# Performance work log

Hardware: AMD Instinct MI355X
Metric: run time of the kernel (lower is better)

## Reference

```python
import jax, jax.numpy as jnp
import numpy as np

B, T, H, LD = 32, 2048, 1024, 1024

def setup_inputs() -> dict:
    key = jax.random.key(0)
    k1, k2, k3, k4, k5 = jax.random.split(key, 5)
    scale = 1.0 / np.sqrt(H)
    return {
        "encoder_hidden": jax.random.normal(k1, (B, T, H), dtype=jnp.float32),
        "decoder_hidden": jax.random.normal(k2, (B, H), dtype=jnp.float32),
        "W1": jax.random.normal(k3, (H, LD), dtype=jnp.float32) * scale,
        "b1": jnp.zeros((LD,), dtype=jnp.float32),
        "W2": jax.random.normal(k4, (H, LD), dtype=jnp.float32) * scale,
        "b2": jnp.zeros((LD,), dtype=jnp.float32),
        "V": jax.random.normal(k5, (LD, 1), dtype=jnp.float32) * (1.0 / np.sqrt(LD)),
        "bV": jnp.zeros((1,), dtype=jnp.float32),
    }

def reference(encoder_hidden, decoder_hidden, W1, b1, W2, b2, V, bV):
    # dec proj: [B, 1, ld]
    dec_w = (decoder_hidden @ W1 + b1)[:, None, :]
    # enc proj: [B, T, ld]
    enc_w = jnp.einsum('bth,hl->btl', encoder_hidden, W2) + b2
    # multiplicative combine (as in source: decoder_Weight * encoder_weight)
    score = jnp.tanh(dec_w * enc_w) @ V + bV          # [B, T, 1]
    attn = jax.nn.softmax(score, axis=1)              # softmax over time
    context = jnp.sum(attn * encoder_hidden, axis=1)  # [B, H]
    return context, attn
```

## Files before the change

### kernel.cpp

```cpp
#include <hip/hip_runtime.h>
#include <hip/hip_bf16.h>
#include <math.h>

#define B_  32
#define T_  2048
#define H_  1024
#define LD_ 1024
#define M_  (B_*T_)

typedef __attribute__((ext_vector_type(8))) short bf16x8;
typedef __attribute__((ext_vector_type(4))) float f32x4;

__device__ __forceinline__ void async_copy16(void* lds, const void* g) {
  __builtin_amdgcn_global_load_lds(
      (const __attribute__((address_space(1))) void*)g,
      (__attribute__((address_space(3))) void*)lds, 16, 0, 0);
}

__global__ void convert_w2(const float* __restrict__ W2, __hip_bfloat16* __restrict__ w2p) {
  int idx = blockIdx.x * 256 + threadIdx.x;
  int kg = idx >> 10, n = idx & 1023;
  __align__(16) __hip_bfloat16 h[8];
#pragma unroll
  for (int j = 0; j < 8; ++j)
    h[j] = __float2bfloat16(W2[(size_t)(kg * 8 + j) * LD_ + n]);
  *reinterpret_cast<uint4*>(&w2p[(size_t)kg * (LD_ * 8) + n * 8]) =
      *reinterpret_cast<const uint4*>(h);
}

__global__ void dec_proj(const float* __restrict__ dec, const float* __restrict__ W1,
                         const float* __restrict__ b1, float* __restrict__ dec_w) {
  __shared__ float sdec[H_];
  int bb = blockIdx.x >> 2;
  int l = (blockIdx.x & 3) * 256 + threadIdx.x;
  for (int i = threadIdx.x; i < H_; i += 256) sdec[i] = dec[bb * H_ + i];
  __syncthreads();
  float a0 = 0.f, a1 = 0.f, a2 = 0.f, a3 = 0.f;
  for (int h = 0; h < H_; h += 4) {
    a0 += sdec[h + 0] * W1[(h + 0) * LD_ + l];
    a1 += sdec[h + 1] * W1[(h + 1) * LD_ + l];
    a2 += sdec[h + 2] * W1[(h + 2) * LD_ + l];
    a3 += sdec[h + 3] * W1[(h + 3) * LD_ + l];
  }
  dec_w[bb * LD_ + l] = (a0 + a1) + (a2 + a3) + b1[l];
}

__global__ __launch_bounds__(256, 2)
void score_gemm(const float* __restrict__ enc,
                const __hip_bfloat16* __restrict__ w2p,
                const float* __restrict__ dec_w,
                const float* __restrict__ b2,
                const float* __restrict__ V,
                float* __restrict__ score) {
  __shared__ __align__(16) __hip_bfloat16 Bsm[2][8][256][8];

  const int tid  = threadIdx.x;
  const int lane = tid & 63;
  const int wave = tid >> 6;
  const int wm = wave >> 1, wn = wave & 1;
  const int bid = blockIdx.y * gridDim.x + blockIdx.x;
  const int swz = (bid & 7) * 256 + (bid >> 3);
  const int mb = swz >> 2, nb = swz & 3;
  const int row0 = mb * 128, col0 = nb * 256;
  const int q = lane >> 4, c15 = lane & 15;

  f32x4 acc[4][8] = {};

  const float* abase = enc + (size_t)(row0 + wm * 64 + c15) * H_ + q * 8;

  float4 ap[4][2];

  auto ALOAD = [&](int k0) {
#pragma unroll
    for (int i = 0; i < 4; ++i) {
      const float4* s = reinterpret_cast<const float4*>(abase + (size_t)i * 16 * H_ + k0);
      ap[i][0] = s[0];
      ap[i][1] = s[1];
    }
  };
  auto ACVT = [&](bf16x8* af) {
#pragma unroll
    for (int i = 0; i < 4; ++i) {
      __align__(16) __hip_bfloat16 h[8];
      h[0] = __float2bfloat16(ap[i][0].x); h[1] = __float2bfloat16(ap[i][0].y);
      h[2] = __float2bfloat16(ap[i][0].z); h[3] = __float2bfloat16(ap[i][0].w);
      h[4] = __float2bfloat16(ap[i][1].x); h[5] = __float2bfloat16(ap[i][1].y);
      h[6] = __float2bfloat16(ap[i][1].z); h[7] = __float2bfloat16(ap[i][1].w);
      af[i] = *reinterpret_cast<const bf16x8*>(h);
    }
  };
  auto GLOADB = [&](int buf, int k0) {
    char* bbase = (char*)&Bsm[buf][0][0][0] + tid * 16;
    const char* gbase = (const char*)w2p + ((size_t)(k0 >> 3)) * (LD_ * 8 * 2)
                        + (size_t)col0 * 16 + tid * 16;
#pragma unroll
    for (int p = 0; p < 8; ++p)
      async_copy16(bbase + p * 4096, gbase + (size_t)p * (LD_ * 8 * 2));
  };

  GLOADB(0, 0);
  ALOAD(0);
  __syncthreads();

  for (int t = 0; t < 16; ++t) {
    const int cur = t & 1;
    const int k0 = t * 64;
    bf16x8 af[4], bfr[8];

    ACVT(af);
    ALOAD(k0 + 32);
    if (t < 15) GLOADB(cur ^ 1, k0 + 64);
#pragma unroll
    for (int j = 0; j < 8; ++j)
      bfr[j] = *reinterpret_cast<const bf16x8*>(&Bsm[cur][q][wn * 128 + j * 16 + c15][0]);
#pragma unroll
    for (int i = 0; i < 4; ++i)
#pragma unroll
      for (int j = 0; j < 8; ++j)
        acc[i][j] = __builtin_amdgcn_mfma_f32_16x16x32_bf16(af[i], bfr[j], acc[i][j], 0, 0, 0);

    ACVT(af);
    if (t < 15) ALOAD(k0 + 64);
#pragma unroll
    for (int j = 0; j < 8; ++j)
      bfr[j] = *reinterpret_cast<const bf16x8*>(&Bsm[cur][q + 4][wn * 128 + j * 16 + c15][0]);
#pragma unroll
    for (int i = 0; i < 4; ++i)
#pragma unroll
      for (int j = 0; j < 8; ++j)
        acc[i][j] = __builtin_amdgcn_mfma_f32_16x16x32_bf16(af[i], bfr[j], acc[i][j], 0, 0, 0);

    __syncthreads();
  }

  const int bb = row0 >> 11;
  float b2v[8], dwv[8], Vv[8];
#pragma unroll
  for (int j = 0; j < 8; ++j) {
    int n = col0 + wn * 128 + j * 16 + c15;
    b2v[j] = b2[n];
    dwv[j] = dec_w[bb * LD_ + n];
    Vv[j]  = V[n];
  }
#pragma unroll
  for (int i = 0; i < 4; ++i) {
#pragma unroll
    for (int r = 0; r < 4; ++r) {
      float v = 0.f;
#pragma unroll
      for (int j = 0; j < 8; ++j) {
        float e = acc[i][j][r] + b2v[j];
        v += tanhf(dwv[j] * e) * Vv[j];
      }
      v += __shfl_xor(v, 1);
      v += __shfl_xor(v, 2);
      v += __shfl_xor(v, 4);
      v += __shfl_xor(v, 8);
      if (c15 == 0) {
        int row = row0 + wm * 64 + i * 16 + q * 4 + r;
        atomicAdd(&score[row], v);
      }
    }
  }
}

__global__ void softmax_k(const float* __restrict__ score, float* __restrict__ attn) {
  int bb = blockIdx.x;
  int tid = threadIdx.x;
  int lane = tid & 63, wave = tid >> 6;
  __shared__ float red[4];
  float v[8];
  float mx = -3.4e38f;
#pragma unroll
  for (int i = 0; i < 8; ++i) {
    v[i] = score[bb * T_ + i * 256 + tid];
    mx = fmaxf(mx, v[i]);
  }
#pragma unroll
  for (int m = 32; m >= 1; m >>= 1) mx = fmaxf(mx, __shfl_xor(mx, m));
  if (lane == 0) red[wave] = mx;
  __syncthreads();
  mx = fmaxf(fmaxf(red[0], red[1]), fmaxf(red[2], red[3]));
  __syncthreads();
  float s = 0.f;
#pragma unroll
  for (int i = 0; i < 8; ++i) { v[i] = __expf(v[i] - mx); s += v[i]; }
#pragma unroll
  for (int m = 32; m >= 1; m >>= 1) s += __shfl_xor(s, m);
  if (lane == 0) red[wave] = s;
  __syncthreads();
  s = red[0] + red[1] + red[2] + red[3];
  float inv = 1.f / s;
#pragma unroll
  for (int i = 0; i < 8; ++i) attn[bb * T_ + i * 256 + tid] = v[i] * inv;
}

__global__ __launch_bounds__(256)
void context_k(const float* __restrict__ enc, const float* __restrict__ attn,
               float* __restrict__ ctx) {
  const int bb = blockIdx.y;
  const int t0 = blockIdx.x * 128;
  __shared__ float sat[128];
  if (threadIdx.x < 128) sat[threadIdx.x] = attn[bb * T_ + t0 + threadIdx.x];
  __syncthreads();
  const float4* base = reinterpret_cast<const float4*>(
      enc + ((size_t)bb * T_ + t0) * H_) + threadIdx.x;
  f32x4 a0 = {}, a1 = {}, a2 = {}, a3 = {};
  for (int t = 0; t < 128; t += 8) {
    float4 v[8];
#pragma unroll
    for (int u = 0; u < 8; ++u) v[u] = base[(size_t)(t + u) * (H_ / 4)];
#pragma unroll
    for (int u = 0; u < 8; ++u) {
      float a = sat[t + u];
      f32x4& d = (u & 2) ? ((u & 1) ? a3 : a2) : ((u & 1) ? a1 : a0);
      d[0] += a * v[u].x; d[1] += a * v[u].y;
      d[2] += a * v[u].z; d[3] += a * v[u].w;
    }
  }
  const int h = threadIdx.x * 4;
  atomicAdd(&ctx[bb * H_ + h + 0], (a0[0] + a1[0]) + (a2[0] + a3[0]));
  atomicAdd(&ctx[bb * H_ + h + 1], (a0[1] + a1[1]) + (a2[1] + a3[1]));
  atomicAdd(&ctx[bb * H_ + h + 2], (a0[2] + a1[2]) + (a2[2] + a3[2]));
  atomicAdd(&ctx[bb * H_ + h + 3], (a0[3] + a1[3]) + (a2[3] + a3[3]));
}

extern "C" void kernel_launch(void* const* d_in, const int* in_sizes, int n_in,
                              void* d_out, int out_size, void* d_ws, size_t ws_size,
                              hipStream_t stream) {
  const float* enc = (const float*)d_in[0];
  const float* dec = (const float*)d_in[1];
  const float* W1  = (const float*)d_in[2];
  const float* b1  = (const float*)d_in[3];
  const float* W2  = (const float*)d_in[4];
  const float* b2  = (const float*)d_in[5];
  const float* V   = (const float*)d_in[6];

  char* ws = (char*)d_ws;
  __hip_bfloat16* w2p = (__hip_bfloat16*)ws;
  float* dec_w = (float*)(ws + (2u << 20));
  float* score = (float*)(ws + (2u << 20) + (128u << 10));

  float* out  = (float*)d_out;
  float* ctx  = out;
  float* attn = out + B_ * H_;

  hipMemsetAsync(score, 0, (size_t)M_ * sizeof(float), stream);
  hipMemsetAsync(ctx, 0, (size_t)B_ * H_ * sizeof(float), stream);

  convert_w2<<<(H_ * LD_ / 8) / 256, 256, 0, stream>>>(W2, w2p);
  dec_proj<<<B_ * 4, 256, 0, stream>>>(dec, W1, b1, dec_w);
  score_gemm<<<dim3(LD_ / 256, M_ / 128), 256, 0, stream>>>(enc, w2p, dec_w, b2, V, score);
  softmax_k<<<B_, 256, 0, stream>>>(score, attn);
  context_k<<<dim3(16, B_), 256, 0, stream>>>(enc, attn, ctx);
}
```

Before: 720.6 us.

## Pre-convert encoder to packed bf16 and load GEMM operands directly from global

Adds a convert_enc pre-pass that writes the encoder activations as bf16 in an MFMA-fragment-friendly packed layout into workspace, when the workspace is large enough. The score GEMM then reads both A and B fragments straight from global memory into registers with a two-stage register double buffer, and drops the LDS staging and per-iteration barriers. The intent is to halve A-side bytes re-read by the four column blocks and to remove in-loop conversion and synchronisation. The cost is an extra full pass over the 256MB encoder tensor plus a 128MB write. Direct global fragment loads may also get less reuse than LDS staging.

```diff
diff --git a/kernel.cpp b/kernel.cpp
--- a/kernel.cpp
+++ b/kernel.cpp
@@ -11,12 +11,6 @@
 typedef __attribute__((ext_vector_type(8))) short bf16x8;
 typedef __attribute__((ext_vector_type(4))) float f32x4;
 
-__device__ __forceinline__ void async_copy16(void* lds, const void* g) {
-  __builtin_amdgcn_global_load_lds(
-      (const __attribute__((address_space(1))) void*)g,
-      (__attribute__((address_space(3))) void*)lds, 16, 0, 0);
-}
-
 __global__ void convert_w2(const float* __restrict__ W2, __hip_bfloat16* __restrict__ w2p) {
   int idx = blockIdx.x * 256 + threadIdx.x;
   int kg = idx >> 10, n = idx & 1023;
@@ -26,6 +20,32 @@
     h[j] = __float2bfloat16(W2[(size_t)(kg * 8 + j) * LD_ + n]);
   *reinterpret_cast<uint4*>(&w2p[(size_t)kg * (LD_ * 8) + n * 8]) =
       *reinterpret_cast<const uint4*>(h);
+}
+
+__global__ __launch_bounds__(256)
+void convert_enc(const float* __restrict__ enc, __hip_bfloat16* __restrict__ encp) {
+  __shared__ __hip_bfloat16 sb[16][H_ + 8];
+  const int rb = blockIdx.x;
+  const int tid = threadIdx.x;
+  const float4* src = reinterpret_cast<const float4*>(enc + (size_t)rb * 16 * H_);
+#pragma unroll
+  for (int p = 0; p < 16; ++p) {
+    int idx = p * 256 + tid;
+    int r = idx >> 8, c4 = idx & 255;
+    float4 f = src[idx];
+    __align__(8) __hip_bfloat16 h[4];
+    h[0] = __float2bfloat16(f.x); h[1] = __float2bfloat16(f.y);
+    h[2] = __float2bfloat16(f.z); h[3] = __float2bfloat16(f.w);
+    *reinterpret_cast<uint2*>(&sb[r][c4 * 4]) = *reinterpret_cast<const uint2*>(h);
+  }
+  __syncthreads();
+  uint4* dst = reinterpret_cast<uint4*>((char*)encp + (size_t)rb * 32768);
+#pragma unroll
+  for (int p = 0; p < 8; ++p) {
+    int c = p * 256 + tid;
+    int kg = c >> 4, rlow = c & 15;
+    dst[c] = *reinterpret_cast<const uint4*>(&sb[rlow][kg * 8]);
+  }
 }
 
 __global__ void dec_proj(const float* __restrict__ dec, const float* __restrict__ W1,
@@ -45,20 +65,20 @@
   dec_w[bb * LD_ + l] = (a0 + a1) + (a2 + a3) + b1[l];
 }
 
+template<bool BF16A>
 __global__ __launch_bounds__(256, 2)
 void score_gemm(const float* __restrict__ enc,
+                const __hip_bfloat16* __restrict__ encp,
                 const __hip_bfloat16* __restrict__ w2p,
                 const float* __restrict__ dec_w,
                 const float* __restrict__ b2,
                 const float* __restrict__ V,
                 float* __restrict__ score) {
-  __shared__ __align__(16) __hip_bfloat16 Bsm[2][8][256][8];
-
   const int tid  = threadIdx.x;
   const int lane = tid & 63;
   const int wave = tid >> 6;
   const int wm = wave >> 1, wn = wave & 1;
-  const int bid = blockIdx.y * gridDim.x + blockIdx.x;
+  const int bid = blockIdx.x;
   const int swz = (bid & 7) * 256 + (bid >> 3);
   const int mb = swz >> 2, nb = swz & 3;
   const int row0 = mb * 128, col0 = nb * 256;
@@ -66,71 +86,63 @@
 
   f32x4 acc[4][8] = {};
 
-  const float* abase = enc + (size_t)(row0 + wm * 64 + c15) * H_ + q * 8;
-
-  float4 ap[4][2];
-
-  auto ALOAD = [&](int k0) {
-#pragma unroll
-    for (int i = 0; i < 4; ++i) {
-      const float4* s = reinterpret_cast<const float4*>(abase + (size_t)i * 16 * H_ + k0);
-      ap[i][0] = s[0];
-      ap[i][1] = s[1];
-    }
-  };
-  auto ACVT = [&](bf16x8* af) {
-#pragma unroll
-    for (int i = 0; i < 4; ++i) {
-      __align__(16) __hip_bfloat16 h[8];
-      h[0] = __float2bfloat16(ap[i][0].x); h[1] = __float2bfloat16(ap[i][0].y);
-      h[2] = __float2bfloat16(ap[i][0].z); h[3] = __float2bfloat16(ap[i][0].w);
-      h[4] = __float2bfloat16(ap[i][1].x); h[5] = __float2bfloat16(ap[i][1].y);
-      h[6] = __float2bfloat16(ap[i][1].z); h[7] = __float2bfloat16(ap[i][1].w);
-      af[i] = *reinterpret_cast<const bf16x8*>(h);
-    }
-  };
-  auto GLOADB = [&](int buf, int k0) {
-    char* bbase = (char*)&Bsm[buf][0][0][0] + tid * 16;
-    const char* gbase = (const char*)w2p + ((size_t)(k0 >> 3)) * (LD_ * 8 * 2)
-                        + (size_t)col0 * 16 + tid * 16;
-#pragma unroll
-    for (int p = 0; p < 8; ++p)
-      async_copy16(bbase + p * 4096, gbase + (size_t)p * (LD_ * 8 * 2));
-  };
-
-  GLOADB(0, 0);
-  ALOAD(0);
-  __syncthreads();
-
-  for (int t = 0; t < 16; ++t) {
-    const int cur = t & 1;
-    const int k0 = t * 64;
-    bf16x8 af[4], bfr[8];
-
-    ACVT(af);
-    ALOAD(k0 + 32);
-    if (t < 15) GLOADB(cur ^ 1, k0 + 64);
+  const __hip_bfloat16* apb = encp + ((size_t)(mb * 8 + wm * 4) * 128 + q) * 128 + c15 * 8;
+  const float* afb = enc + (size_t)(row0 + wm * 64 + c15) * H_ + q * 8;
+  const __hip_bfloat16* bpb = w2p + ((size_t)q * LD_ + col0 + wn * 128 + c15) * 8;
+
+  bf16x8 a0[4], b0[8], a1[4], b1[8];
+  float4 p0[8], p1[8];
+
+  auto LOADB = [&](bf16x8* bf, int ks) {
+    const __hip_bfloat16* p = bpb + (size_t)ks * (4 * LD_ * 8);
 #pragma unroll
     for (int j = 0; j < 8; ++j)
-      bfr[j] = *reinterpret_cast<const bf16x8*>(&Bsm[cur][q][wn * 128 + j * 16 + c15][0]);
+      bf[j] = *reinterpret_cast<const bf16x8*>(p + j * (16 * 8));
+  };
+  auto LOADA = [&](bf16x8* af, float4* ap, int ks) {
+    if constexpr (BF16A) {
+      const __hip_bfloat16* p = apb + (size_t)ks * (4 * 128);
+#pragma unroll
+      for (int i = 0; i < 4; ++i)
+        af[i] = *reinterpret_cast<const bf16x8*>(p + (size_t)i * (128 * 128));
+    } else {
+#pragma unroll
+      for (int i = 0; i < 4; ++i) {
+        const float4* s = reinterpret_cast<const float4*>(afb + (size_t)i * 16 * H_ + ks * 32);
+        ap[i * 2]     = s[0];
+        ap[i * 2 + 1] = s[1];
+      }
+    }
+  };
+  auto CVTA = [&](bf16x8* af, const float4* ap) {
+    if constexpr (!BF16A) {
+#pragma unroll
+      for (int i = 0; i < 4; ++i) {
+        __align__(16) __hip_bfloat16 h[8];
+        h[0] = __float2bfloat16(ap[i*2].x);   h[1] = __float2bfloat16(ap[i*2].y);
+        h[2] = __float2bfloat16(ap[i*2].z);   h[3] = __float2bfloat16(ap[i*2].w);
+        h[4] = __float2bfloat16(ap[i*2+1].x); h[5] = __float2bfloat16(ap[i*2+1].y);
+        h[6] = __float2bfloat16(ap[i*2+1].z); h[7] = __float2bfloat16(ap[i*2+1].w);
+        af[i] = *reinterpret_cast<const bf16x8*>(h);
+      }
+    }
+  };
+  auto MFMA = [&](const bf16x8* af, const bf16x8* bf) {
 #pragma unroll
     for (int i = 0; i < 4; ++i)
 #pragma unroll
       for (int j = 0; j < 8; ++j)
-        acc[i][j] = __builtin_amdgcn_mfma_f32_16x16x32_bf16(af[i], bfr[j], acc[i][j], 0, 0, 0);
-
-    ACVT(af);
-    if (t < 15) ALOAD(k0 + 64);
-#pragma unroll
-    for (int j = 0; j < 8; ++j)
-      bfr[j] = *reinterpret_cast<const bf16x8*>(&Bsm[cur][q + 4][wn * 128 + j * 16 + c15][0]);
-#pragma unroll
-    for (int i = 0; i < 4; ++i)
-#pragma unroll
-      for (int j = 0; j < 8; ++j)
-        acc[i][j] = __builtin_amdgcn_mfma_f32_16x16x32_bf16(af[i], bfr[j], acc[i][j], 0, 0, 0);
-
-    __syncthreads();
+        acc[i][j] = __builtin_amdgcn_mfma_f32_16x16x32_bf16(af[i], bf[j], acc[i][j], 0, 0, 0);
+  };
+
+  LOADA(a0, p0, 0); LOADB(b0, 0);
+  for (int it = 0; it < 16; ++it) {
+    LOADA(a1, p1, 2 * it + 1); LOADB(b1, 2 * it + 1);
+    CVTA(a0, p0);
+    MFMA(a0, b0);
+    if (it < 15) { LOADA(a0, p0, 2 * it + 2); LOADB(b0, 2 * it + 2); }
+    CVTA(a1, p1);
+    MFMA(a1, b1);
   }
 
   const int bb = row0 >> 11;
@@ -240,6 +252,10 @@
   __hip_bfloat16* w2p = (__hip_bfloat16*)ws;
   float* dec_w = (float*)(ws + (2u << 20));
   float* score = (float*)(ws + (2u << 20) + (128u << 10));
+  const size_t encp_off = (2u << 20) + (384u << 10);
+  __hip_bfloat16* encp = (__hip_bfloat16*)(ws + encp_off);
+  const size_t need = encp_off + (size_t)M_ * H_ * 2;
+  const bool bf16a = ws_size >= need;
 
   float* out  = (float*)d_out;
   float* ctx  = out;
@@ -248,9 +264,15 @@
   hipMemsetAsync(score, 0, (size_t)M_ * sizeof(float), stream);
   hipMemsetAsync(ctx, 0, (size_t)B_ * H_ * sizeof(float), stream);
 
+  if (bf16a) convert_enc<<<M_ / 16, 256, 0, stream>>>(enc, encp);
   convert_w2<<<(H_ * LD_ / 8) / 256, 256, 0, stream>>>(W2, w2p);
   dec_proj<<<B_ * 4, 256, 0, stream>>>(dec, W1, b1, dec_w);
-  score_gemm<<<dim3(LD_ / 256, M_ / 128), 256, 0, stream>>>(enc, w2p, dec_w, b2, V, score);
+  if (bf16a)
+    score_gemm<true><<<(M_ / 128) * (LD_ / 256), 256, 0, stream>>>(
+        enc, encp, w2p, dec_w, b2, V, score);
+  else
+    score_gemm<false><<<(M_ / 128) * (LD_ / 256), 256, 0, stream>>>(
+        enc, encp, w2p, dec_w, b2, V, score);
   softmax_k<<<B_, 256, 0, stream>>>(score, attn);
   context_k<<<dim3(16, B_), 256, 0, stream>>>(enc, attn, ctx);
 }
```

After: 721.9 us. No clear change (+0.2%).
